# Optimization experiments

Measured on AMD Instinct MI355X. Metric: run time of the kernel, lower is better.

## Reference

```python
import jax, jax.numpy as jnp
import numpy as np

N, E, B = 40000, 640000, 256
F_IN, H, D = 128, 128, 128  # num_node_features, hidden_dim, last_dim
EPS = 1e-5


def sage_conv(x, src, dst, Wl, bl, Wr, num_nodes):
    # PyG SAGEConv (mean aggr): out = lin_l(mean_j x_j) + lin_r(x)
    msg = x[src]                                            # [E, d] gather
    agg = jax.ops.segment_sum(msg, dst, num_segments=num_nodes)
    cnt = jax.ops.segment_sum(jnp.ones((src.shape[0],), x.dtype), dst,
                              num_segments=num_nodes)
    mean = agg / jnp.maximum(cnt, 1.0)[:, None]
    return mean @ Wl.T + bl + x @ Wr.T


def bn_eval(x, g, b, rm, rv):
    return g * (x - rm) * jax.lax.rsqrt(rv + EPS) + b


def lstm_cell(inp, h, c, Wih, Whh, bih, bhh):
    gates = inp @ Wih.T + h @ Whh.T + bih + bhh             # [B, 4D]
    i, f, g, o = jnp.split(gates, 4, axis=-1)
    c = jax.nn.sigmoid(f) * c + jax.nn.sigmoid(i) * jnp.tanh(g)
    h = jax.nn.sigmoid(o) * jnp.tanh(c)
    return h, c


def set2set(x, batch, Wih, Whh, bih, bhh, num_graphs, steps=3):
    d = x.shape[1]
    q_star = jnp.zeros((num_graphs, 2 * d), x.dtype)
    h = jnp.zeros((num_graphs, d), x.dtype)
    c = jnp.zeros((num_graphs, d), x.dtype)
    for _ in range(steps):
        h, c = lstm_cell(q_star, h, c, Wih, Whh, bih, bhh)
        q = h                                               # [B, D]
        e = jnp.sum(x * q[batch], axis=-1)                  # [N]
        emax = jax.ops.segment_max(e, batch, num_segments=num_graphs)
        a = jnp.exp(e - emax[batch])
        denom = jax.ops.segment_sum(a, batch, num_segments=num_graphs)
        a = a / denom[batch]
        r = jax.ops.segment_sum(a[:, None] * x, batch, num_segments=num_graphs)
        q_star = jnp.concatenate([q, r], axis=-1)
    return q_star


def setup_inputs() -> dict:
    key = jax.random.key(0)
    ks = jax.random.split(key, 20)
    x = jax.random.normal(ks[0], (N, F_IN), jnp.float32)
    edge_index = jax.random.randint(ks[1], (2, E), 0, N)
    batch = jnp.sort(jax.random.randint(ks[2], (N,), 0, B))
    s1, s2, sd = 1.0 / np.sqrt(F_IN), 1.0 / np.sqrt(H), 1.0 / np.sqrt(D)
    return {
        "x": x, "edge_index": edge_index, "batch": batch,
        "W1l": jax.random.normal(ks[3], (H, F_IN)) * s1,
        "b1l": jnp.zeros((H,)),
        "W1r": jax.random.normal(ks[4], (H, F_IN)) * s1,
        "g1": jnp.ones((H,)), "beta1": jnp.zeros((H,)),
        "rm1": jax.random.normal(ks[5], (H,)) * 0.1,
        "rv1": jax.random.uniform(ks[6], (H,), minval=0.5, maxval=1.5),
        "W2l": jax.random.normal(ks[7], (D, H)) * s2,
        "b2l": jnp.zeros((D,)),
        "W2r": jax.random.normal(ks[8], (D, H)) * s2,
        "g2": jnp.ones((D,)), "beta2": jnp.zeros((D,)),
        "rm2": jax.random.normal(ks[9], (D,)) * 0.1,
        "rv2": jax.random.uniform(ks[10], (D,), minval=0.5, maxval=1.5),
        "Wih": jax.random.normal(ks[11], (4 * D, 2 * D)) * sd,
        "Whh": jax.random.normal(ks[12], (4 * D, D)) * sd,
        "bih": jnp.zeros((4 * D,)), "bhh": jnp.zeros((4 * D,)),
        "Wp": jax.random.normal(ks[13], (D, 2 * D)) * sd,
        "bp": jnp.zeros((D,)),
    }


def reference(x, edge_index, batch, W1l, b1l, W1r, g1, beta1, rm1, rv1,
              W2l, b2l, W2r, g2, beta2, rm2, rv2, Wih, Whh, bih, bhh, Wp, bp):
    src, dst = edge_index[0], edge_index[1]
    num_nodes = x.shape[0]
    h1 = jax.nn.relu(bn_eval(sage_conv(x, src, dst, W1l, b1l, W1r, num_nodes),
                             g1, beta1, rm1, rv1))
    # dropout is identity in eval mode
    h2 = jax.nn.relu(bn_eval(sage_conv(h1, src, dst, W2l, b2l, W2r, num_nodes),
                             g2, beta2, rm2, rv2))
    q_star = set2set(h2, batch, Wih, Whh, bih, bhh, B, steps=3)  # [B, 2D]
    return q_star @ Wp.T + bp                                    # [B, D]
```

## Files before the change

### kernel.cpp

```cpp
#include <hip/hip_runtime.h>
#include <hip/hip_bf16.h>
#include <math.h>

#define NN 40000
#define NE 640000
#define NG 256
#define FD 128
#define SLOT 96

typedef __attribute__((ext_vector_type(8))) short bf16x8;
typedef __attribute__((ext_vector_type(4))) float f32x4;

__device__ __forceinline__ float sigf(float x) { return 1.f / (1.f + __expf(-x)); }
__device__ __forceinline__ unsigned short f2b(float f) {
    unsigned int u = __float_as_uint(f);
    return (unsigned short)((u + 0x7FFFu + ((u >> 16) & 1u)) >> 16);
}
__device__ __forceinline__ float b2f(unsigned int u16) {
    return __uint_as_float(u16 << 16);
}

__global__ void k_setup(const int* __restrict__ ei, const int* __restrict__ batch,
                        int* __restrict__ gptr, int* __restrict__ dcnt,
                        int* __restrict__ srcs,
                        const float* __restrict__ W1l, const float* __restrict__ W1r,
                        const float* __restrict__ W2l, const float* __restrict__ W2r,
                        unsigned short* __restrict__ Wb,
                        const float* __restrict__ Wihf, const float* __restrict__ Whhf,
                        unsigned short* __restrict__ Wb2) {
    int blk = blockIdx.x, t = threadIdx.x;
    if (blk < 625) {
        int i = blk * 256 + t;
        int4 s4 = ((const int4*)ei)[i];
        int4 d4 = ((const int4*)(ei + NE))[i];
        int p0 = atomicAdd(&dcnt[d4.x], 1);
        if (p0 < SLOT) srcs[d4.x * SLOT + p0] = s4.x;
        int p1 = atomicAdd(&dcnt[d4.y], 1);
        if (p1 < SLOT) srcs[d4.y * SLOT + p1] = s4.y;
        int p2 = atomicAdd(&dcnt[d4.z], 1);
        if (p2 < SLOT) srcs[d4.z * SLOT + p2] = s4.z;
        int p3 = atomicAdd(&dcnt[d4.w], 1);
        if (p3 < SLOT) srcs[d4.w * SLOT + p3] = s4.w;
    } else if (blk < 782) {
        int i = (blk - 625) * 256 + t;
        if (i >= NN) return;
        int b = batch[i];
        int pb = (i == 0) ? -1 : batch[i - 1];
        for (int g = pb + 1; g <= b; g++) gptr[g] = i;
        if (i == NN - 1)
            for (int g = b + 1; g <= NG; g++) gptr[g] = NN;
    } else if (blk < 846) {
        int j4 = (blk - 782) * 256 + t;
        int seg = j4 >> 12, off4 = j4 & 4095;
        const float* W = (seg == 0) ? W1l : (seg == 1) ? W1r : (seg == 2) ? W2l : W2r;
        float4 v = ((const float4*)W)[off4];
        ushort4 o;
        o.x = f2b(v.x); o.y = f2b(v.y); o.z = f2b(v.z); o.w = f2b(v.w);
        *(ushort4*)(Wb + (size_t)j4 * 4) = o;
    } else {
        int j4 = (blk - 846) * 256 + t;
        float4 v;
        size_t off;
        if (j4 < 32768) {
            int r = j4 >> 6, f4 = j4 & 63;
            int c = f4 >> 1, h = f4 & 1;
            v = ((const float4*)Wihf)[j4];
            off = ((size_t)c * 512 + r) * 8 + h * 4;
        } else {
            int jj = j4 - 32768;
            int r = jj >> 5, f4 = jj & 31;
            int c = f4 >> 1, h = f4 & 1;
            v = ((const float4*)Whhf)[jj];
            off = (size_t)512 * 256 + ((size_t)c * 512 + r) * 8 + h * 4;
        }
        ushort4 o;
        o.x = f2b(v.x); o.y = f2b(v.y); o.z = f2b(v.z); o.w = f2b(v.w);
        *(ushort4*)(Wb2 + off) = o;
    }
}

__global__ __launch_bounds__(256) void k_mm(
    const void* __restrict__ Av, int a_fp32,
    const unsigned short* __restrict__ W,
    unsigned short* __restrict__ C)
{
    __shared__ unsigned short Ws[128 * 128];
    int t = threadIdx.x;
    int nh = blockIdx.x & 1;
    int mblk = blockIdx.x >> 1;
    {
        const uint4* Wg = (const uint4*)(W + nh * 128 * 128);
#pragma unroll
        for (int i = 0; i < 8; i++) {
            int f = i * 256 + t;
            int row = f >> 4, c = f & 15;
            int cs = c ^ (row & 15);
            *(uint4*)&Ws[row * 128 + cs * 8] = Wg[f];
        }
    }
    __syncthreads();
    int w = t >> 6, lane = t & 63;
    int ln = lane & 15, quad = lane >> 4;
    int m0 = mblk * 64 + w * 16;
    bf16x8 a[4];
    if (a_fp32) {
        const float* Arow = (const float*)Av + (size_t)(m0 + ln) * 128;
#pragma unroll
        for (int ks = 0; ks < 4; ks++) {
            float4 u0 = *(const float4*)(Arow + ks * 32 + quad * 8);
            float4 u1 = *(const float4*)(Arow + ks * 32 + quad * 8 + 4);
            unsigned short tmp[8];
            tmp[0] = f2b(u0.x); tmp[1] = f2b(u0.y); tmp[2] = f2b(u0.z); tmp[3] = f2b(u0.w);
            tmp[4] = f2b(u1.x); tmp[5] = f2b(u1.y); tmp[6] = f2b(u1.z); tmp[7] = f2b(u1.w);
            a[ks] = *(const bf16x8*)tmp;
        }
    } else {
        const unsigned short* Arow = (const unsigned short*)Av + (size_t)(m0 + ln) * 128;
#pragma unroll
        for (int ks = 0; ks < 4; ks++)
            a[ks] = *(const bf16x8*)(Arow + ks * 32 + quad * 8);
    }
    for (int nt = 0; nt < 8; nt++) {
        int n0 = nt * 16;
        int row = n0 + ln;
        f32x4 acc = {0.f, 0.f, 0.f, 0.f};
#pragma unroll
        for (int ks = 0; ks < 4; ks++) {
            int c = ks * 4 + quad;
            bf16x8 b = *(const bf16x8*)&Ws[row * 128 + (c ^ (row & 15)) * 8];
            acc = __builtin_amdgcn_mfma_f32_16x16x32_bf16(a[ks], b, acc, 0, 0, 0);
        }
        size_t base = (size_t)(m0 + quad * 4) * 256 + nh * 128 + n0 + ln;
#pragma unroll
        for (int r = 0; r < 4; r++)
            C[base + (size_t)r * 256] = f2b(acc[r]);
    }
}

__global__ __launch_bounds__(256) void k_gather2(
    const unsigned short* __restrict__ C, const int* __restrict__ srcs,
    const int* __restrict__ dcnt,
    const float* __restrict__ bl,
    const float* __restrict__ gam, const float* __restrict__ bet,
    const float* __restrict__ rme, const float* __restrict__ rva,
    unsigned short* __restrict__ H)
{
    int t = threadIdx.x;
    int qw = t >> 4, l4 = t & 15;
    int node = blockIdx.x * 16 + qw;
    int deg = dcnt[node];
    int cnt = (deg < SLOT) ? deg : SLOT;
    int s0 = node * SLOT, e0 = s0 + cnt;
    const uint4* C4 = (const uint4*)C;
    float ac[8];
#pragma unroll
    for (int k = 0; k < 8; k++) ac[k] = 0.f;
    int i = s0;
    for (; i + 7 < e0; i += 8) {
        uint4 v0 = C4[(size_t)srcs[i]     * 32 + l4];
        uint4 v1 = C4[(size_t)srcs[i + 1] * 32 + l4];
        uint4 v2 = C4[(size_t)srcs[i + 2] * 32 + l4];
        uint4 v3 = C4[(size_t)srcs[i + 3] * 32 + l4];
        uint4 v4 = C4[(size_t)srcs[i + 4] * 32 + l4];
        uint4 v5 = C4[(size_t)srcs[i + 5] * 32 + l4];
        uint4 v6 = C4[(size_t)srcs[i + 6] * 32 + l4];
        uint4 v7 = C4[(size_t)srcs[i + 7] * 32 + l4];
        ac[0] += b2f(v0.x & 0xFFFFu) + b2f(v1.x & 0xFFFFu) + b2f(v2.x & 0xFFFFu) + b2f(v3.x & 0xFFFFu)
               + b2f(v4.x & 0xFFFFu) + b2f(v5.x & 0xFFFFu) + b2f(v6.x & 0xFFFFu) + b2f(v7.x & 0xFFFFu);
        ac[1] += b2f(v0.x >> 16) + b2f(v1.x >> 16) + b2f(v2.x >> 16) + b2f(v3.x >> 16)
               + b2f(v4.x >> 16) + b2f(v5.x >> 16) + b2f(v6.x >> 16) + b2f(v7.x >> 16);
        ac[2] += b2f(v0.y & 0xFFFFu) + b2f(v1.y & 0xFFFFu) + b2f(v2.y & 0xFFFFu) + b2f(v3.y & 0xFFFFu)
               + b2f(v4.y & 0xFFFFu) + b2f(v5.y & 0xFFFFu) + b2f(v6.y & 0xFFFFu) + b2f(v7.y & 0xFFFFu);
        ac[3] += b2f(v0.y >> 16) + b2f(v1.y >> 16) + b2f(v2.y >> 16) + b2f(v3.y >> 16)
               + b2f(v4.y >> 16) + b2f(v5.y >> 16) + b2f(v6.y >> 16) + b2f(v7.y >> 16);
        ac[4] += b2f(v0.z & 0xFFFFu) + b2f(v1.z & 0xFFFFu) + b2f(v2.z & 0xFFFFu) + b2f(v3.z & 0xFFFFu)
               + b2f(v4.z & 0xFFFFu) + b2f(v5.z & 0xFFFFu) + b2f(v6.z & 0xFFFFu) + b2f(v7.z & 0xFFFFu);
        ac[5] += b2f(v0.z >> 16) + b2f(v1.z >> 16) + b2f(v2.z >> 16) + b2f(v3.z >> 16)
               + b2f(v4.z >> 16) + b2f(v5.z >> 16) + b2f(v6.z >> 16) + b2f(v7.z >> 16);
        ac[6] += b2f(v0.w & 0xFFFFu) + b2f(v1.w & 0xFFFFu) + b2f(v2.w & 0xFFFFu) + b2f(v3.w & 0xFFFFu)
               + b2f(v4.w & 0xFFFFu) + b2f(v5.w & 0xFFFFu) + b2f(v6.w & 0xFFFFu) + b2f(v7.w & 0xFFFFu);
        ac[7] += b2f(v0.w >> 16) + b2f(v1.w >> 16) + b2f(v2.w >> 16) + b2f(v3.w >> 16)
               + b2f(v4.w >> 16) + b2f(v5.w >> 16) + b2f(v6.w >> 16) + b2f(v7.w >> 16);
    }
    for (; i < e0; i++) {
        uint4 v = C4[(size_t)srcs[i] * 32 + l4];
        ac[0] += b2f(v.x & 0xFFFFu); ac[1] += b2f(v.x >> 16);
        ac[2] += b2f(v.y & 0xFFFFu); ac[3] += b2f(v.y >> 16);
        ac[4] += b2f(v.z & 0xFFFFu); ac[5] += b2f(v.z >> 16);
        ac[6] += b2f(v.w & 0xFFFFu); ac[7] += b2f(v.w >> 16);
    }
    float inv = 1.0f / fmaxf((float)deg, 1.0f);
    uint4 yr = C4[(size_t)node * 32 + 16 + l4];
    float yo[8];
    yo[0] = b2f(yr.x & 0xFFFFu); yo[1] = b2f(yr.x >> 16);
    yo[2] = b2f(yr.y & 0xFFFFu); yo[3] = b2f(yr.y >> 16);
    yo[4] = b2f(yr.z & 0xFFFFu); yo[5] = b2f(yr.z >> 16);
    yo[6] = b2f(yr.w & 0xFFFFu); yo[7] = b2f(yr.w >> 16);
    float4 ga = ((const float4*)gam)[l4 * 2],     gb = ((const float4*)gam)[l4 * 2 + 1];
    float4 va = ((const float4*)rva)[l4 * 2],     vb = ((const float4*)rva)[l4 * 2 + 1];
    float4 ma = ((const float4*)rme)[l4 * 2],     mb = ((const float4*)rme)[l4 * 2 + 1];
    float4 ba = ((const float4*)bet)[l4 * 2],     bb = ((const float4*)bet)[l4 * 2 + 1];
    float4 la = ((const float4*)bl)[l4 * 2],      lb = ((const float4*)bl)[l4 * 2 + 1];
    float g[8] = {ga.x, ga.y, ga.z, ga.w, gb.x, gb.y, gb.z, gb.w};
    float rv[8] = {va.x, va.y, va.z, va.w, vb.x, vb.y, vb.z, vb.w};
    float rm[8] = {ma.x, ma.y, ma.z, ma.w, mb.x, mb.y, mb.z, mb.w};
    float bt[8] = {ba.x, ba.y, ba.z, ba.w, bb.x, bb.y, bb.z, bb.w};
    float lv[8] = {la.x, la.y, la.z, la.w, lb.x, lb.y, lb.z, lb.w};
    unsigned short o[8];
#pragma unroll
    for (int k = 0; k < 8; k++) {
        float y = ac[k] * inv + yo[k] + lv[k];
        float z = g[k] * rsqrtf(rv[k] + 1e-5f) * (y - rm[k]) + bt[k];
        o[k] = f2b(fmaxf(z, 0.f));
    }
    *(uint4*)(H + (size_t)node * 128 + l4 * 8) = *(const uint4*)o;
}

__global__ __launch_bounds__(1024) void k_s2s(
    const unsigned short* __restrict__ h2, const int* __restrict__ gptr,
    const float* __restrict__ bih, const float* __restrict__ bhh,
    const unsigned short* __restrict__ Wihb, const unsigned short* __restrict__ Whhb,
    const float* __restrict__ Wp, const float* __restrict__ bp,
    float* __restrict__ out)
{
    int b = blockIdx.x, t = threadIdx.x;
    int wave = t >> 6, lane = t & 63;
    __shared__ float hs[FD];
    __shared__ float qstar[2 * FD];
    __shared__ float gates_s[512];
    __shared__ float es[512];
    __shared__ float wm[16], wd[16], red[16][FD];
    float creg = 0.f;
    int start = gptr[b], end = gptr[b + 1];
    int seg = end - start;
    const unsigned int* H2 = (const unsigned int*)h2;

    for (int step = 0; step < 3; step++) {
        if (step == 0) {
            if (t < FD) {
                float ig = bih[t] + bhh[t];
                float gg = bih[2 * FD + t] + bhh[2 * FD + t];
                float og = bih[3 * FD + t] + bhh[3 * FD + t];
                float c = sigf(ig) * tanhf(gg);
                float h = sigf(og) * tanhf(c);
                creg = c; hs[t] = h;
            }
        } else {
            if (t < 512) {
                float acc = bih[t] + bhh[t];
                const uint4* wi = (const uint4*)Wihb;
                for (int k = 0; k < 32; k++) {
                    uint4 u = wi[k * 512 + t];
                    const float* q = &qstar[k * 8];
                    acc += b2f(u.x & 0xFFFFu)*q[0] + b2f(u.x >> 16)*q[1]
                         + b2f(u.y & 0xFFFFu)*q[2] + b2f(u.y >> 16)*q[3]
                         + b2f(u.z & 0xFFFFu)*q[4] + b2f(u.z >> 16)*q[5]
                         + b2f(u.w & 0xFFFFu)*q[6] + b2f(u.w >> 16)*q[7];
                }
                const uint4* wh = (const uint4*)Whhb;
                for (int k = 0; k < 16; k++) {
                    uint4 u = wh[k * 512 + t];
                    const float* hq = &hs[k * 8];
                    acc += b2f(u.x & 0xFFFFu)*hq[0] + b2f(u.x >> 16)*hq[1]
                         + b2f(u.y & 0xFFFFu)*hq[2] + b2f(u.y >> 16)*hq[3]
                         + b2f(u.z & 0xFFFFu)*hq[4] + b2f(u.z >> 16)*hq[5]
                         + b2f(u.w & 0xFFFFu)*hq[6] + b2f(u.w >> 16)*hq[7];
                }
                gates_s[t] = acc;
            }
            __syncthreads();
            if (t < FD) {
                float ig = gates_s[t], fg = gates_s[FD + t];
                float gg = gates_s[2 * FD + t], og = gates_s[3 * FD + t];
                float c = sigf(fg) * creg + sigf(ig) * tanhf(gg);
                float h = sigf(og) * tanhf(c);
                creg = c; hs[t] = h;
            }
        }
        __syncthreads();

        float2 q = ((const float2*)hs)[lane];
        float rx = 0.f, ry = 0.f, dw = 0.f;

        if (seg <= 512) {
            float mw = -INFINITY;
            for (int n = start + wave; n < end; n += 16) {
                unsigned int u = H2[(size_t)n * 64 + lane];
                float vx = b2f(u & 0xFFFFu), vy = b2f(u >> 16);
                float e = vx * q.x + vy * q.y;
#pragma unroll
                for (int off = 32; off; off >>= 1) e += __shfl_xor(e, off);
                if (lane == 0) es[n - start] = e;
                mw = fmaxf(mw, e);
            }
            if (lane == 0) wm[wave] = mw;
            __syncthreads();
            float M = wm[0];
#pragma unroll
            for (int k = 1; k < 16; k++) M = fmaxf(M, wm[k]);
            for (int n = start + wave; n < end; n += 16) {
                unsigned int u = H2[(size_t)n * 64 + lane];
                float vx = b2f(u & 0xFFFFu), vy = b2f(u >> 16);
                float a = __expf(es[n - start] - M);
                rx += a * vx; ry += a * vy; dw += a;
            }
            red[wave][2 * lane] = rx;
            red[wave][2 * lane + 1] = ry;
            if (lane == 0) wd[wave] = dw;
        } else {
            float mw = -INFINITY;
            for (int n = start + wave; n < end; n += 16) {
                unsigned int u = H2[(size_t)n * 64 + lane];
                float vx = b2f(u & 0xFFFFu), vy = b2f(u >> 16);
                float e = vx * q.x + vy * q.y;
#pragma unroll
                for (int off = 32; off; off >>= 1) e += __shfl_xor(e, off);
                float mn = fmaxf(mw, e);
                float corr = __expf(mw - mn);
                float a = __expf(e - mn);
                rx = rx * corr + a * vx;
                ry = ry * corr + a * vy;
                dw = dw * corr + a;
                mw = mn;
            }
            if (lane == 0) wm[wave] = mw;
            __syncthreads();
            float M = wm[0];
#pragma unroll
            for (int k = 1; k < 16; k++) M = fmaxf(M, wm[k]);
            float cr = (M == -INFINITY) ? 0.f : __expf(mw - M);
            red[wave][2 * lane] = rx * cr;
            red[wave][2 * lane + 1] = ry * cr;
            if (lane == 0) wd[wave] = dw * cr;
        }
        __syncthreads();
        if (t < FD) {
            float r = 0.f, den = 0.f;
#pragma unroll
            for (int k = 0; k < 16; k++) { r += red[k][t]; den += wd[k]; }
            float rn = (den > 0.f) ? r / den : 0.f;
            qstar[t] = hs[t];
            qstar[FD + t] = rn;
        }
        __syncthreads();
    }

    if (t < FD) {
        const float4* w4 = (const float4*)(Wp + (size_t)t * 256);
        const float4* q4 = (const float4*)qstar;
        float acc = bp[t];
        for (int k = 0; k < 64; k++) {
            float4 wv = w4[k], qv = q4[k];
            acc += qv.x*wv.x + qv.y*wv.y + qv.z*wv.z + qv.w*wv.w;
        }
        out[(size_t)b * FD + t] = acc;
    }
}

__global__ void k_zero_out(float* __restrict__ out, int n) {
    int i = blockIdx.x * blockDim.x + threadIdx.x;
    if (i < n) out[i] = 0.f;
}

extern "C" void kernel_launch(void* const* d_in, const int* in_sizes, int n_in,
                              void* d_out, int out_size, void* d_ws, size_t ws_size,
                              hipStream_t stream) {
    const float* x   = (const float*)d_in[0];
    const int*  ei    = (const int*)d_in[1];
    const int*  batch = (const int*)d_in[2];
    const float* W1l = (const float*)d_in[3];
    const float* b1l = (const float*)d_in[4];
    const float* W1r = (const float*)d_in[5];
    const float* g1  = (const float*)d_in[6];
    const float* be1 = (const float*)d_in[7];
    const float* rm1 = (const float*)d_in[8];
    const float* rv1 = (const float*)d_in[9];
    const float* W2l = (const float*)d_in[10];
    const float* b2l = (const float*)d_in[11];
    const float* W2r = (const float*)d_in[12];
    const float* g2  = (const float*)d_in[13];
    const float* be2 = (const float*)d_in[14];
    const float* rm2 = (const float*)d_in[15];
    const float* rv2 = (const float*)d_in[16];
    const float* Wih = (const float*)d_in[17];
    const float* Whh = (const float*)d_in[18];
    const float* bih = (const float*)d_in[19];
    const float* bhh = (const float*)d_in[20];
    const float* Wp  = (const float*)d_in[21];
    const float* bp  = (const float*)d_in[22];
    float* out = (float*)d_out;

    auto al = [](size_t s) { return (s + 255) & ~(size_t)255; };
    size_t off_dcnt = 0;
    size_t off_gptr = off_dcnt + al((size_t)NN * 4);
    size_t off_srcs = off_gptr + al((size_t)(NG + 1) * 4);
    size_t off_h2b  = off_srcs + al((size_t)NN * SLOT * 4);
    size_t off_h1b  = off_h2b  + al((size_t)NN * FD * 2);
    size_t off_Wb   = off_h1b  + al((size_t)NN * FD * 2);
    size_t off_Wb2  = off_Wb   + al((size_t)2 * 256 * 128 * 2);
    size_t off_C    = off_Wb2  + al((size_t)(512 * 256 + 512 * 128) * 2);
    size_t need     = off_C    + al((size_t)NN * 256 * 2);

    if (ws_size < need) {
        k_zero_out<<<(out_size + 255) / 256, 256, 0, stream>>>(out, out_size);
        return;
    }

    char* p = (char*)d_ws;
    int* dcnt    = (int*)(p + off_dcnt);
    int* gptr    = (int*)(p + off_gptr);
    int* srcs    = (int*)(p + off_srcs);
    unsigned short* h2b = (unsigned short*)(p + off_h2b);
    unsigned short* h1b = (unsigned short*)(p + off_h1b);
    unsigned short* Wb  = (unsigned short*)(p + off_Wb);
    unsigned short* Wb2 = (unsigned short*)(p + off_Wb2);
    unsigned short* C   = (unsigned short*)(p + off_C);

    hipMemsetAsync(dcnt, 0, (size_t)NN * 4, stream);

    k_setup<<<1038, 256, 0, stream>>>(ei, batch, gptr, dcnt, srcs,
                                      W1l, W1r, W2l, W2r, Wb, Wih, Whh, Wb2);

    k_mm<<<1250, 256, 0, stream>>>(x, 1, Wb, C);
    k_gather2<<<NN / 16, 256, 0, stream>>>(C, srcs, dcnt, b1l, g1, be1, rm1, rv1, h1b);

    k_mm<<<1250, 256, 0, stream>>>(h1b, 0, Wb + 32768, C);
    k_gather2<<<NN / 16, 256, 0, stream>>>(C, srcs, dcnt, b2l, g2, be2, rm2, rv2, h2b);

    k_s2s<<<NG, 1024, 0, stream>>>(h2b, gptr, bih, bhh,
                                   Wb2, Wb2 + 512 * 256, Wp, bp, out);
}
```

Measured before the change: 261.1 us.

## Fuse setup work into first GEMM launch with interleaved heterogeneous blocks

Merges the setup kernel (CSR-style edge bucketing, graph pointers, weight bf16 conversion) with the first layer's GEMM into one launch, interleaving setup blocks with GEMM blocks. The first GEMM now converts W1l/W1r from fp32 to bf16 directly into shared memory, so it no longer waits on a separate conversion pass. This removes one kernel launch and the dependency barrier between setup and GEMM, letting atomic-heavy bucketing overlap with tensor-core work. In exchange, every GEMM block redoes the fp32 weight conversion, and the shared-memory allocation now also applies to setup blocks, which may lower occupancy.

```diff
diff --git a/kernel.cpp b/kernel.cpp
--- a/kernel.cpp
+++ b/kernel.cpp
@@ -20,67 +20,127 @@
     return __uint_as_float(u16 << 16);
 }
 
-__global__ void k_setup(const int* __restrict__ ei, const int* __restrict__ batch,
-                        int* __restrict__ gptr, int* __restrict__ dcnt,
-                        int* __restrict__ srcs,
-                        const float* __restrict__ W1l, const float* __restrict__ W1r,
-                        const float* __restrict__ W2l, const float* __restrict__ W2r,
-                        unsigned short* __restrict__ Wb,
-                        const float* __restrict__ Wihf, const float* __restrict__ Whhf,
-                        unsigned short* __restrict__ Wb2) {
-    int blk = blockIdx.x, t = threadIdx.x;
-    if (blk < 625) {
-        int i = blk * 256 + t;
-        int4 s4 = ((const int4*)ei)[i];
-        int4 d4 = ((const int4*)(ei + NE))[i];
-        int p0 = atomicAdd(&dcnt[d4.x], 1);
-        if (p0 < SLOT) srcs[d4.x * SLOT + p0] = s4.x;
-        int p1 = atomicAdd(&dcnt[d4.y], 1);
-        if (p1 < SLOT) srcs[d4.y * SLOT + p1] = s4.y;
-        int p2 = atomicAdd(&dcnt[d4.z], 1);
-        if (p2 < SLOT) srcs[d4.z * SLOT + p2] = s4.z;
-        int p3 = atomicAdd(&dcnt[d4.w], 1);
-        if (p3 < SLOT) srcs[d4.w * SLOT + p3] = s4.w;
-    } else if (blk < 782) {
-        int i = (blk - 625) * 256 + t;
-        if (i >= NN) return;
-        int b = batch[i];
-        int pb = (i == 0) ? -1 : batch[i - 1];
-        for (int g = pb + 1; g <= b; g++) gptr[g] = i;
-        if (i == NN - 1)
-            for (int g = b + 1; g <= NG; g++) gptr[g] = NN;
-    } else if (blk < 846) {
-        int j4 = (blk - 782) * 256 + t;
-        int seg = j4 >> 12, off4 = j4 & 4095;
-        const float* W = (seg == 0) ? W1l : (seg == 1) ? W1r : (seg == 2) ? W2l : W2r;
-        float4 v = ((const float4*)W)[off4];
-        ushort4 o;
-        o.x = f2b(v.x); o.y = f2b(v.y); o.z = f2b(v.z); o.w = f2b(v.w);
-        *(ushort4*)(Wb + (size_t)j4 * 4) = o;
-    } else {
-        int j4 = (blk - 846) * 256 + t;
-        float4 v;
-        size_t off;
-        if (j4 < 32768) {
-            int r = j4 >> 6, f4 = j4 & 63;
-            int c = f4 >> 1, h = f4 & 1;
-            v = ((const float4*)Wihf)[j4];
-            off = ((size_t)c * 512 + r) * 8 + h * 4;
+__global__ __launch_bounds__(256) void k_fused1(
+    const float* __restrict__ A,
+    const float* __restrict__ W1l, const float* __restrict__ W1r,
+    unsigned short* __restrict__ C,
+    const int* __restrict__ ei, const int* __restrict__ batch,
+    int* __restrict__ gptr, int* __restrict__ dcnt, int* __restrict__ srcs,
+    const float* __restrict__ W2l, const float* __restrict__ W2r,
+    unsigned short* __restrict__ Wb,
+    const float* __restrict__ Wihf, const float* __restrict__ Whhf,
+    unsigned short* __restrict__ Wb2)
+{
+    __shared__ unsigned short Ws[128 * 128];
+    int bid = blockIdx.x, t = threadIdx.x;
+
+    if ((bid < 2012) && (bid & 1)) {
+        int sidx = bid >> 1;
+        if (sidx < 625) {
+            int i = sidx * 256 + t;
+            int4 s4 = ((const int4*)ei)[i];
+            int4 d4 = ((const int4*)(ei + NE))[i];
+            int p0 = atomicAdd(&dcnt[d4.x], 1);
+            if (p0 < SLOT) srcs[d4.x * SLOT + p0] = s4.x;
+            int p1 = atomicAdd(&dcnt[d4.y], 1);
+            if (p1 < SLOT) srcs[d4.y * SLOT + p1] = s4.y;
+            int p2 = atomicAdd(&dcnt[d4.z], 1);
+            if (p2 < SLOT) srcs[d4.z * SLOT + p2] = s4.z;
+            int p3 = atomicAdd(&dcnt[d4.w], 1);
+            if (p3 < SLOT) srcs[d4.w * SLOT + p3] = s4.w;
+        } else if (sidx < 782) {
+            int i = (sidx - 625) * 256 + t;
+            if (i >= NN) return;
+            int b = batch[i];
+            int pb = (i == 0) ? -1 : batch[i - 1];
+            for (int g = pb + 1; g <= b; g++) gptr[g] = i;
+            if (i == NN - 1)
+                for (int g = b + 1; g <= NG; g++) gptr[g] = NN;
+        } else if (sidx < 814) {
+            int j4 = (sidx - 782) * 256 + t;
+            int seg = j4 >> 12, off4 = j4 & 4095;
+            const float* W = seg ? W2r : W2l;
+            float4 v = ((const float4*)W)[off4];
+            ushort4 o;
+            o.x = f2b(v.x); o.y = f2b(v.y); o.z = f2b(v.z); o.w = f2b(v.w);
+            *(ushort4*)(Wb + (size_t)j4 * 4) = o;
         } else {
-            int jj = j4 - 32768;
-            int r = jj >> 5, f4 = jj & 31;
-            int c = f4 >> 1, h = f4 & 1;
-            v = ((const float4*)Whhf)[jj];
-            off = (size_t)512 * 256 + ((size_t)c * 512 + r) * 8 + h * 4;
-        }
-        ushort4 o;
-        o.x = f2b(v.x); o.y = f2b(v.y); o.z = f2b(v.z); o.w = f2b(v.w);
-        *(ushort4*)(Wb2 + off) = o;
-    }
-}
-
-__global__ __launch_bounds__(256) void k_mm(
-    const void* __restrict__ Av, int a_fp32,
+            int j4 = (sidx - 814) * 256 + t;
+            float4 v;
+            size_t off;
+            if (j4 < 32768) {
+                int r = j4 >> 6, f4 = j4 & 63;
+                int c = f4 >> 1, h = f4 & 1;
+                v = ((const float4*)Wihf)[j4];
+                off = ((size_t)c * 512 + r) * 8 + h * 4;
+            } else {
+                int jj = j4 - 32768;
+                int r = jj >> 5, f4 = jj & 31;
+                int c = f4 >> 1, h = f4 & 1;
+                v = ((const float4*)Whhf)[jj];
+                off = (size_t)512 * 256 + ((size_t)c * 512 + r) * 8 + h * 4;
+            }
+            ushort4 o;
+            o.x = f2b(v.x); o.y = f2b(v.y); o.z = f2b(v.z); o.w = f2b(v.w);
+            *(ushort4*)(Wb2 + off) = o;
+        }
+        return;
+    }
+
+    int mblk2 = (bid < 2012) ? (bid >> 1) : (bid - 1006);
+    int nh = mblk2 & 1;
+    int mblk = mblk2 >> 1;
+    {
+        const float* Wsrc = nh ? W1r : W1l;
+#pragma unroll
+        for (int i = 0; i < 8; i++) {
+            int f = i * 256 + t;
+            int row = f >> 4, c = f & 15;
+            float4 u0 = *(const float4*)(Wsrc + row * 128 + c * 8);
+            float4 u1 = *(const float4*)(Wsrc + row * 128 + c * 8 + 4);
+            unsigned short tmp[8];
+            tmp[0] = f2b(u0.x); tmp[1] = f2b(u0.y); tmp[2] = f2b(u0.z); tmp[3] = f2b(u0.w);
+            tmp[4] = f2b(u1.x); tmp[5] = f2b(u1.y); tmp[6] = f2b(u1.z); tmp[7] = f2b(u1.w);
+            int cs = c ^ (row & 15);
+            *(uint4*)&Ws[row * 128 + cs * 8] = *(const uint4*)tmp;
+        }
+    }
+    __syncthreads();
+    int w = t >> 6, lane = t & 63;
+    int ln = lane & 15, quad = lane >> 4;
+    int m0 = mblk * 64 + w * 16;
+    bf16x8 a[4];
+    {
+        const float* Arow = A + (size_t)(m0 + ln) * 128;
+#pragma unroll
+        for (int ks = 0; ks < 4; ks++) {
+            float4 u0 = *(const float4*)(Arow + ks * 32 + quad * 8);
+            float4 u1 = *(const float4*)(Arow + ks * 32 + quad * 8 + 4);
+            unsigned short tmp[8];
+            tmp[0] = f2b(u0.x); tmp[1] = f2b(u0.y); tmp[2] = f2b(u0.z); tmp[3] = f2b(u0.w);
+            tmp[4] = f2b(u1.x); tmp[5] = f2b(u1.y); tmp[6] = f2b(u1.z); tmp[7] = f2b(u1.w);
+            a[ks] = *(const bf16x8*)tmp;
+        }
+    }
+    for (int nt = 0; nt < 8; nt++) {
+        int n0 = nt * 16;
+        int row = n0 + ln;
+        f32x4 acc = {0.f, 0.f, 0.f, 0.f};
+#pragma unroll
+        for (int ks = 0; ks < 4; ks++) {
+            int c = ks * 4 + quad;
+            bf16x8 b = *(const bf16x8*)&Ws[row * 128 + (c ^ (row & 15)) * 8];
+            acc = __builtin_amdgcn_mfma_f32_16x16x32_bf16(a[ks], b, acc, 0, 0, 0);
+        }
+        size_t base = (size_t)(m0 + quad * 4) * 256 + nh * 128 + n0 + ln;
+#pragma unroll
+        for (int r = 0; r < 4; r++)
+            C[base + (size_t)r * 256] = f2b(acc[r]);
+    }
+}
+
+__global__ __launch_bounds__(256) void k_mm_bf16(
+    const unsigned short* __restrict__ A,
     const unsigned short* __restrict__ W,
     unsigned short* __restrict__ C)
 {
@@ -103,19 +163,8 @@
     int ln = lane & 15, quad = lane >> 4;
     int m0 = mblk * 64 + w * 16;
     bf16x8 a[4];
-    if (a_fp32) {
-        const float* Arow = (const float*)Av + (size_t)(m0 + ln) * 128;
-#pragma unroll
-        for (int ks = 0; ks < 4; ks++) {
-            float4 u0 = *(const float4*)(Arow + ks * 32 + quad * 8);
-            float4 u1 = *(const float4*)(Arow + ks * 32 + quad * 8 + 4);
-            unsigned short tmp[8];
-            tmp[0] = f2b(u0.x); tmp[1] = f2b(u0.y); tmp[2] = f2b(u0.z); tmp[3] = f2b(u0.w);
-            tmp[4] = f2b(u1.x); tmp[5] = f2b(u1.y); tmp[6] = f2b(u1.z); tmp[7] = f2b(u1.w);
-            a[ks] = *(const bf16x8*)tmp;
-        }
-    } else {
-        const unsigned short* Arow = (const unsigned short*)Av + (size_t)(m0 + ln) * 128;
+    {
+        const unsigned short* Arow = A + (size_t)(m0 + ln) * 128;
 #pragma unroll
         for (int ks = 0; ks < 4; ks++)
             a[ks] = *(const bf16x8*)(Arow + ks * 32 + quad * 8);
@@ -397,7 +446,7 @@
     size_t off_h2b  = off_srcs + al((size_t)NN * SLOT * 4);
     size_t off_h1b  = off_h2b  + al((size_t)NN * FD * 2);
     size_t off_Wb   = off_h1b  + al((size_t)NN * FD * 2);
-    size_t off_Wb2  = off_Wb   + al((size_t)2 * 256 * 128 * 2);
+    size_t off_Wb2  = off_Wb   + al((size_t)256 * 128 * 2);
     size_t off_C    = off_Wb2  + al((size_t)(512 * 256 + 512 * 128) * 2);
     size_t need     = off_C    + al((size_t)NN * 256 * 2);
 
@@ -418,13 +467,12 @@
 
     hipMemsetAsync(dcnt, 0, (size_t)NN * 4, stream);
 
-    k_setup<<<1038, 256, 0, stream>>>(ei, batch, gptr, dcnt, srcs,
-                                      W1l, W1r, W2l, W2r, Wb, Wih, Whh, Wb2);
-
-    k_mm<<<1250, 256, 0, stream>>>(x, 1, Wb, C);
+    k_fused1<<<2256, 256, 0, stream>>>(x, W1l, W1r, C,
+                                       ei, batch, gptr, dcnt, srcs,
+                                       W2l, W2r, Wb, Wih, Whh, Wb2);
     k_gather2<<<NN / 16, 256, 0, stream>>>(C, srcs, dcnt, b1l, g1, be1, rm1, rv1, h1b);
 
-    k_mm<<<1250, 256, 0, stream>>>(h1b, 0, Wb + 32768, C);
+    k_mm_bf16<<<1250, 256, 0, stream>>>(h1b, Wb, C);
     k_gather2<<<NN / 16, 256, 0, stream>>>(C, srcs, dcnt, b2l, g2, be2, rm2, rv2, h2b);
 
     k_s2s<<<NG, 1024, 0, stream>>>(h2b, gptr, bih, bhh,
```

New measurement: 246.2 us. 5.7% less time.
